# Kernel optimization log

Measured on AMD Instinct MI355X. Metric: run time of the kernel, lower is better.

## Reference

```python
import jax, jax.numpy as jnp
import numpy as np

jax.config.update("jax_enable_x64", True)  # original numpy code runs in float64

B, T, D = 8, 1600, 64
WINDOW, TAK_DIM, TAK_TAU = 50, 3, 1
N_RADII, N_BINS, N_FEAT = 20, 20, 8
N = WINDOW - (TAK_DIM - 1) * TAK_TAU          # 48 points per Takens cloud
L_CAP = N * (N - 1) // 2                      # hard upper bound on beta_1
_OFF = np.where(~np.eye(N, dtype=bool))      # static off-diagonal indices
EIG_TOL = 1e-6


def setup_inputs():
    key = jax.random.key(0)
    k1, k2, k3 = jax.random.split(key, 3)
    latent_seq = jax.random.normal(k1, (B, T, D), dtype=jnp.float32)
    W = jax.random.normal(k2, (N_FEAT, N_FEAT), dtype=jnp.float32) / np.sqrt(N_FEAT)
    b = jax.random.normal(k3, (N_FEAT,), dtype=jnp.float32) * 0.01
    return {"latent_seq": latent_seq, "W": W, "b": b}


def _pairwise(X):
    sq = jnp.sum(X * X, axis=1)
    D2 = sq[:, None] + sq[None, :] - 2.0 * (X @ X.T)
    return jnp.sqrt(jnp.maximum(D2, 0.0))


def _prim_deaths(Dm):
    # MST edge weights == H0 death times of single-linkage (Kruskal) for generic weights
    BIG = jnp.asarray(1e30, Dm.dtype)
    def step(carry, _):
        in_tree, mind = carry
        cand = jnp.where(in_tree, BIG, mind)
        j = jnp.argmin(cand)
        w = cand[j]
        in_tree = in_tree.at[j].set(True)
        mind = jnp.minimum(mind, Dm[j])
        return (in_tree, mind), w
    in0 = jnp.zeros((N,), bool).at[0].set(True)
    _, deaths = jax.lax.scan(step, (in0, Dm[0]), None, length=N - 1)
    return deaths


def _entropy(lifetimes, valid):
    lt = jnp.where(valid & (lifetimes > 0), lifetimes, 0.0)
    s = jnp.sum(lt)
    p = lt / jnp.where(s > 0, s, 1.0)
    ent = -jnp.sum(jnp.where(p > 0, p * jnp.log(p), 0.0))
    return jnp.where(s > 0, ent, 0.0)


def _landscape_integral(births, deaths, valid):
    # k=1 persistence landscape on N_BINS grid, summarized by its mean
    has = jnp.any(valid)
    t0 = jnp.where(has, jnp.min(jnp.where(valid, births, jnp.inf)), 0.0)
    t1 = jnp.where(has, jnp.max(jnp.where(valid, deaths, -jnp.inf)), 1.0)
    t = jnp.linspace(t0, t1, N_BINS)
    tent = jnp.minimum(t[:, None] - births[None, :], deaths[None, :] - t[:, None])
    tent = jnp.where(valid[None, :], tent, -jnp.inf)
    lam = jnp.maximum(jnp.max(tent, axis=1), 0.0)
    return jnp.where(has, jnp.mean(lam), 0.0)


def _window_features(cloud):
    Dm = _pairwise(cloud)                       # (N, N)
    vals = Dm[_OFF]                             # all positive off-diagonal distances
    radii = jnp.percentile(vals, jnp.linspace(10.0, 90.0, N_RADII))
    r_med = jnp.median(vals)

    # ---- H0 (exact): single-linkage deaths via vectorized Prim MST
    deaths0 = _prim_deaths(Dm)                  # (N-1,)
    valid0 = jnp.ones(deaths0.shape, bool)
    beta0 = jnp.sum(deaths0 > r_med).astype(Dm.dtype)
    ent0 = _entropy(deaths0, valid0)
    maxp0 = jnp.max(deaths0)
    land0 = _landscape_integral(jnp.zeros_like(deaths0), deaths0, valid0)

    # ---- H1 (spectral proxy): Laplacian eigendecomposition per filtration radius
    offmask = ~jnp.eye(N, dtype=bool)
    A = (Dm[None, :, :] <= radii[:, None, None]) & offmask   # (R, N, N)
    Af = A.astype(jnp.float64)
    deg = Af.sum(-1)                             # (R, N)
    ii = jnp.arange(N)
    Lap = (-Af).at[:, ii, ii].set(deg)
    eig = jnp.linalg.eigvalsh(Lap)               # (R, N), ascending
    comps = jnp.sum(eig < EIG_TOL, axis=1)
    edges = jnp.sum(A, axis=(1, 2)) // 2
    beta1 = jnp.maximum(0, edges - N + comps)    # (R,) int, prev_beta1 starts at 0

    # LIFO birth/death pair tracking == per-level run extraction of (beta1 >= l)
    lev = jnp.arange(1, L_CAP + 1)
    Alev = beta1[None, :] >= lev[:, None]                      # (L_CAP, R)
    prev = jnp.concatenate([jnp.zeros((L_CAP, 1), bool), Alev[:, :-1]], axis=1)
    starts = Alev & ~prev
    ends = (~Alev) & prev                                      # finite deaths only
    step_idx = jnp.arange(N_RADII)
    last_start = jax.lax.cummax(jnp.where(starts, step_idx, -1), axis=1)
    births1 = radii[jnp.clip(last_start, 0)]                   # (L_CAP, R)
    deathr1 = jnp.broadcast_to(radii[None, :], (L_CAP, N_RADII))
    life1 = deathr1 - births1
    beta1_med = jnp.sum(ends & (births1 <= r_med) & (r_med < deathr1)).astype(Dm.dtype)
    ent1 = _entropy(life1.ravel(), ends.ravel())
    maxp1 = jnp.max(jnp.where(ends, life1, 0.0))
    land1 = _landscape_integral(births1.ravel(), deathr1.ravel(), ends.ravel())

    return jnp.stack([beta0, beta1_med, ent0, ent1, maxp0, maxp1, land0, land1]).astype(jnp.float32)


def _topo_features(latent_seq):
    series = jnp.linalg.norm(latent_seq, axis=-1)   # (B, T) scalar series per step
    nw = T // WINDOW
    wins = series[:, : nw * WINDOW].reshape(B * nw, WINDOW)
    tak = np.arange(N)[:, None] + np.arange(TAK_DIM)[None, :] * TAK_TAU
    clouds = wins[:, tak]                           # (B*nw, N, TAK_DIM) Takens embedding
    feats = jax.vmap(_window_features)(clouds)      # (B*nw, 8)
    return feats.reshape(B, nw, N_FEAT)


def reference(latent_seq, W, b):
    feats = _topo_features(latent_seq)              # torch version is @no_grad
    return feats @ W.T + b                          # feature_proj: Linear(8, 8)
```

## Files before the change

kernel.cpp:

```cpp
#include <hip/hip_runtime.h>
#include <math.h>

#define T_LEN 1600
#define D_DIM 64
#define WIN   50
#define NPT   48
#define NPAIR 1128
#define VPL   18
#define K_MED 563

template <typename F>
__device__ __forceinline__ int dpp_red63(int v, F op) {
    int t;
    t = __builtin_amdgcn_update_dpp(v, v, 0xb1, 0xf, 0xf, false); v = op(v, t);
    t = __builtin_amdgcn_update_dpp(v, v, 0x4e, 0xf, 0xf, false); v = op(v, t);
    t = __builtin_amdgcn_update_dpp(v, v, 0x114, 0xf, 0xe, false); v = op(v, t);
    t = __builtin_amdgcn_update_dpp(v, v, 0x118, 0xf, 0xc, false); v = op(v, t);
    t = __builtin_amdgcn_update_dpp(v, v, 0x142, 0xa, 0xf, false); v = op(v, t);
    t = __builtin_amdgcn_update_dpp(v, v, 0x143, 0xc, 0xf, false); v = op(v, t);
    return v;
}
__device__ __forceinline__ float wave_fmin_bc(float v) {
    int r = dpp_red63(__float_as_int(v), [](int a, int b) {
        return __float_as_int(fminf(__int_as_float(a), __int_as_float(b))); });
    return __int_as_float(__builtin_amdgcn_readlane(r, 63));
}
__device__ __forceinline__ float wave_fmax_bc(float v) {
    int r = dpp_red63(__float_as_int(v), [](int a, int b) {
        return __float_as_int(fmaxf(__int_as_float(a), __int_as_float(b))); });
    return __int_as_float(__builtin_amdgcn_readlane(r, 63));
}
__device__ __forceinline__ float wave_fadd_bc(float v) {
    int r = dpp_red63(__float_as_int(v), [](int a, int b) {
        return __float_as_int(__fadd_rn(__int_as_float(a), __int_as_float(b))); });
    return __int_as_float(__builtin_amdgcn_readlane(r, 63));
}
__device__ __forceinline__ unsigned wave_umin_bc(unsigned v) {
    int r = dpp_red63((int)v, [](int a, int b) {
        unsigned ua = (unsigned)a, ub = (unsigned)b;
        return (int)(ua < ub ? ua : ub); });
    return (unsigned)__builtin_amdgcn_readlane(r, 63);
}

__global__ __launch_bounds__(256)
void topo_feats_kernel(const float* __restrict__ latent,
                       const float* __restrict__ W,
                       const float* __restrict__ bvec,
                       float* __restrict__ out)
{
    __shared__ float s_series[WIN];
    __shared__ float s_sq[NPT];
    __shared__ float s_D[NPT * NPT];
    __shared__ float s_med;

    const int w   = blockIdx.x;
    const int bb  = w >> 5;
    const int kk  = w & 31;
    const int tid = threadIdx.x;

    if (tid < 64) {
        const int lane = tid;
        float x0 = 0.0f;
        if (lane < WIN) {
            const float* p = latent + ((size_t)bb * T_LEN + (size_t)kk * WIN + lane) * D_DIM;
            float r[8];
#pragma unroll
            for (int q = 0; q < 8; ++q) r[q] = 0.0f;
#pragma unroll
            for (int i = 0; i < D_DIM; i += 8)
#pragma unroll
                for (int q = 0; q < 8; ++q)
                    r[q] = __fadd_rn(r[q], __fmul_rn(p[i + q], p[i + q]));
            float ss = __fadd_rn(__fadd_rn(__fadd_rn(r[0], r[1]), __fadd_rn(r[2], r[3])),
                                 __fadd_rn(__fadd_rn(r[4], r[5]), __fadd_rn(r[6], r[7])));
            x0 = sqrtf(ss);
        }
        float x1 = __shfl_down(x0, 1);
        float x2 = __shfl_down(x0, 2);
        if (lane < WIN) s_series[lane] = x0;
        if (lane < NPT)
            s_sq[lane] = __fadd_rn(__fadd_rn(__fmul_rn(x0, x0), __fmul_rn(x1, x1)),
                                   __fmul_rn(x2, x2));
    }
    __syncthreads();

    for (int e = tid; e < NPT * NPT; e += 256) {
        int i = e / NPT, j = e - i * NPT;
        float dot = fmaf(s_series[i + 2], s_series[j + 2],
                    fmaf(s_series[i + 1], s_series[j + 1],
                         __fmul_rn(s_series[i], s_series[j])));
        float d2 = __fsub_rn(__fadd_rn(s_sq[i], s_sq[j]), __fmul_rn(2.0f, dot));
        s_D[i * NPT + j] = sqrtf(fmaxf(d2, 0.0f));
    }
    __syncthreads();

    const int wv   = tid >> 6;
    const int lane = tid & 63;
    float dreg = 0.0f;

    if (wv == 0) {
        bool  intree = (lane == 0);
        float mind   = (lane < NPT) ? s_D[lane] : 1e30f;
        for (int it = 0; it < NPT - 1; ++it) {
            float cand = (intree || lane >= NPT) ? 1e30f : mind;
            float wmin = wave_fmin_bc(cand);
            if (lane == it) dreg = wmin;
            unsigned long long m = __ballot(cand == wmin);
            int id = __ffsll(m) - 1;
            if (lane == id) intree = true;
            if (lane < NPT) mind = fminf(mind, s_D[id * NPT + lane]);
        }
    } else if (wv == 1) {
        unsigned ub[VPL];
#pragma unroll
        for (int r = 0; r < VPL; ++r) {
            int e = lane + 64 * r;
            unsigned v = 0xFFFFFFFFu;
            if (e < NPAIR) {
                int i = (int)((95.0f - sqrtf((float)(9025 - 8 * e))) * 0.5f);
                i = (i < 0) ? 0 : ((i > NPT - 2) ? NPT - 2 : i);
                int offi = (i * (95 - i)) >> 1;
                int offn = ((i + 1) * (94 - i)) >> 1;
                if (e >= offn)      { ++i; offi = offn; }
                else if (e < offi)  { --i; offi = (i * (95 - i)) >> 1; }
                int j = i + 1 + (e - offi);
                v = __float_as_uint(s_D[i * NPT + j]);
            }
            ub[r] = v;
        }
        unsigned lo = 0;
        for (int bit = 30; bit >= 0; --bit) {
            unsigned probe = lo | (1u << bit);
            int c = 0;
#pragma unroll
            for (int r = 0; r < VPL; ++r)
                c += __popcll(__ballot(ub[r] < probe));
            if (c <= K_MED) lo = probe;
        }
        const unsigned v0 = lo;
        int cle = 0; unsigned mn = 0xFFFFFFFFu;
#pragma unroll
        for (int r = 0; r < VPL; ++r) {
            cle += __popcll(__ballot(ub[r] <= v0));
            if (ub[r] > v0 && ub[r] < mn) mn = ub[r];
        }
        mn = wave_umin_bc(mn);
        unsigned v1 = (cle >= K_MED + 2) ? v0 : mn;
        if (lane == 0)
            s_med = __fadd_rn(__fmul_rn(0.5f, __uint_as_float(v0)),
                              __fmul_rn(0.5f, __uint_as_float(v1)));
    }
    __syncthreads();

    if (wv == 0) {
        const float rmed = s_med;
        const bool  isd  = (lane < NPT - 1);
        const float d    = isd ? dreg : 0.0f;

        float beta0 = (float)__popcll(__ballot(isd && (d > rmed)));
        float mx    = wave_fmax_bc(isd ? d : -INFINITY);

        float sv = (isd && d > 0.0f) ? d : 0.0f;
        float ss = wave_fadd_bc(sv);

        float p    = sv / ss;
        float term = (p > 0.0f) ? -p * logf(p) : 0.0f;
        float ent  = wave_fadd_bc(term);

        float step = mx / 19.0f;
        float t    = step * (float)lane;
        float lam  = (lane < 20) ? fmaxf(fminf(t, mx - t), 0.0f) : 0.0f;
        float land = wave_fadd_bc(lam) * (1.0f / 20.0f);

        if (lane < 8) {
            float o = bvec[lane]
                    + beta0 * W[lane * 8 + 0]
                    + ent   * W[lane * 8 + 2]
                    + mx    * W[lane * 8 + 4]
                    + land  * W[lane * 8 + 6];
            out[w * 8 + lane] = o;
        }
    }
}

extern "C" void kernel_launch(void* const* d_in, const int* in_sizes, int n_in,
                              void* d_out, int out_size, void* d_ws, size_t ws_size,
                              hipStream_t stream)
{
    const float* latent = (const float*)d_in[0];
    const float* W      = (const float*)d_in[1];
    const float* bvec   = (const float*)d_in[2];
    float*       out    = (float*)d_out;

    topo_feats_kernel<<<dim3(256), dim3(256), 0, stream>>>(latent, W, bvec, out);

    (void)in_sizes; (void)n_in; (void)out_size; (void)d_ws; (void)ws_size;
}
```

Before: 19.00 us.

## Shrink block to two waves, cache distance column in registers for Prim

Block size drops from 256 to 128 threads, because only two wavefronts ever did useful work in the later phases. The distance matrix fill is unrolled to match. Each Prim lane preloads its column of the distance matrix into registers and picks the row with a 48-way switch instead of reading LDS every iteration. The W and b loads are hoisted to kernel start and the latent norm uses float4 loads. The switch may become a long branch chain or an indexed-register access, and the extra registers may spill, which could cancel the saving on LDS latency.

```diff
diff --git a/kernel.cpp b/kernel.cpp
--- a/kernel.cpp
+++ b/kernel.cpp
@@ -42,7 +42,9 @@
     return (unsigned)__builtin_amdgcn_readlane(r, 63);
 }
 
-__global__ __launch_bounds__(256)
+#define CDV(k) case k: dv = colD[k]; break;
+
+__global__ __launch_bounds__(128)
 void topo_feats_kernel(const float* __restrict__ latent,
                        const float* __restrict__ W,
                        const float* __restrict__ bvec,
@@ -53,24 +55,42 @@
     __shared__ float s_D[NPT * NPT];
     __shared__ float s_med;
 
-    const int w   = blockIdx.x;
-    const int bb  = w >> 5;
-    const int kk  = w & 31;
-    const int tid = threadIdx.x;
-
-    if (tid < 64) {
-        const int lane = tid;
+    const int w    = blockIdx.x;
+    const int bb   = w >> 5;
+    const int kk   = w & 31;
+    const int tid  = threadIdx.x;
+    const int wv   = tid >> 6;
+    const int lane = tid & 63;
+
+    float pb = 0.0f, pw0 = 0.0f, pw2 = 0.0f, pw4 = 0.0f, pw6 = 0.0f;
+    if (wv == 0 && lane < 8) {
+        pb  = bvec[lane];
+        pw0 = W[lane * 8 + 0];
+        pw2 = W[lane * 8 + 2];
+        pw4 = W[lane * 8 + 4];
+        pw6 = W[lane * 8 + 6];
+    }
+
+    if (wv == 0) {
         float x0 = 0.0f;
         if (lane < WIN) {
-            const float* p = latent + ((size_t)bb * T_LEN + (size_t)kk * WIN + lane) * D_DIM;
+            const float4* p4 = (const float4*)(latent +
+                ((size_t)bb * T_LEN + (size_t)kk * WIN + lane) * D_DIM);
             float r[8];
 #pragma unroll
             for (int q = 0; q < 8; ++q) r[q] = 0.0f;
 #pragma unroll
-            for (int i = 0; i < D_DIM; i += 8)
-#pragma unroll
-                for (int q = 0; q < 8; ++q)
-                    r[q] = __fadd_rn(r[q], __fmul_rn(p[i + q], p[i + q]));
+            for (int i = 0; i < 16; i += 2) {
+                float4 a = p4[i], b = p4[i + 1];
+                r[0] = __fadd_rn(r[0], __fmul_rn(a.x, a.x));
+                r[1] = __fadd_rn(r[1], __fmul_rn(a.y, a.y));
+                r[2] = __fadd_rn(r[2], __fmul_rn(a.z, a.z));
+                r[3] = __fadd_rn(r[3], __fmul_rn(a.w, a.w));
+                r[4] = __fadd_rn(r[4], __fmul_rn(b.x, b.x));
+                r[5] = __fadd_rn(r[5], __fmul_rn(b.y, b.y));
+                r[6] = __fadd_rn(r[6], __fmul_rn(b.z, b.z));
+                r[7] = __fadd_rn(r[7], __fmul_rn(b.w, b.w));
+            }
             float ss = __fadd_rn(__fadd_rn(__fadd_rn(r[0], r[1]), __fadd_rn(r[2], r[3])),
                                  __fadd_rn(__fadd_rn(r[4], r[5]), __fadd_rn(r[6], r[7])));
             x0 = sqrtf(ss);
@@ -84,7 +104,9 @@
     }
     __syncthreads();
 
-    for (int e = tid; e < NPT * NPT; e += 256) {
+#pragma unroll
+    for (int k = 0; k < NPT * NPT / 128; ++k) {
+        int e = tid + 128 * k;
         int i = e / NPT, j = e - i * NPT;
         float dot = fmaf(s_series[i + 2], s_series[j + 2],
                     fmaf(s_series[i + 1], s_series[j + 1],
@@ -94,13 +116,17 @@
     }
     __syncthreads();
 
-    const int wv   = tid >> 6;
-    const int lane = tid & 63;
     float dreg = 0.0f;
 
     if (wv == 0) {
+        float colD[NPT];
+        const int src = (lane < NPT) ? lane : NPT - 1;
+#pragma unroll
+        for (int j = 0; j < NPT; ++j) colD[j] = s_D[j * NPT + src];
+
         bool  intree = (lane == 0);
-        float mind   = (lane < NPT) ? s_D[lane] : 1e30f;
+        float mind   = colD[0];
+#pragma unroll 1
         for (int it = 0; it < NPT - 1; ++it) {
             float cand = (intree || lane >= NPT) ? 1e30f : mind;
             float wmin = wave_fmin_bc(cand);
@@ -108,9 +134,19 @@
             unsigned long long m = __ballot(cand == wmin);
             int id = __ffsll(m) - 1;
             if (lane == id) intree = true;
-            if (lane < NPT) mind = fminf(mind, s_D[id * NPT + lane]);
-        }
-    } else if (wv == 1) {
+            float dv;
+            switch (id) {
+                CDV(0)  CDV(1)  CDV(2)  CDV(3)  CDV(4)  CDV(5)  CDV(6)  CDV(7)
+                CDV(8)  CDV(9)  CDV(10) CDV(11) CDV(12) CDV(13) CDV(14) CDV(15)
+                CDV(16) CDV(17) CDV(18) CDV(19) CDV(20) CDV(21) CDV(22) CDV(23)
+                CDV(24) CDV(25) CDV(26) CDV(27) CDV(28) CDV(29) CDV(30) CDV(31)
+                CDV(32) CDV(33) CDV(34) CDV(35) CDV(36) CDV(37) CDV(38) CDV(39)
+                CDV(40) CDV(41) CDV(42) CDV(43) CDV(44) CDV(45) CDV(46) CDV(47)
+                default: dv = 1e30f; break;
+            }
+            mind = fminf(mind, dv);
+        }
+    } else {
         unsigned ub[VPL];
 #pragma unroll
         for (int r = 0; r < VPL; ++r) {
@@ -173,11 +209,7 @@
         float land = wave_fadd_bc(lam) * (1.0f / 20.0f);
 
         if (lane < 8) {
-            float o = bvec[lane]
-                    + beta0 * W[lane * 8 + 0]
-                    + ent   * W[lane * 8 + 2]
-                    + mx    * W[lane * 8 + 4]
-                    + land  * W[lane * 8 + 6];
+            float o = pb + beta0 * pw0 + ent * pw2 + mx * pw4 + land * pw6;
             out[w * 8 + lane] = o;
         }
     }
@@ -192,7 +224,7 @@
     const float* bvec   = (const float*)d_in[2];
     float*       out    = (float*)d_out;
 
-    topo_feats_kernel<<<dim3(256), dim3(256), 0, stream>>>(latent, W, bvec, out);
+    topo_feats_kernel<<<dim3(256), dim3(128), 0, stream>>>(latent, W, bvec, out);
 
     (void)in_sizes; (void)n_in; (void)out_size; (void)d_ws; (void)ws_size;
 }
```

After: 21.07 us. 10.9% more time.
